# Performance work log

Measured on AMD Instinct MI355X. Metric: run time of the kernel, lower is better.

## Reference

```python
import jax, jax.numpy as jnp
import numpy as np

N_NODES = 50000
N_EDGES = 800000
VOCAB = 4096          # node_emb_size
EMB_DIM = 128         # node_emb_dim
HIDDEN = 128          # hidden_dim -> layer1 out = 2*HIDDEN
N_POS = 1024


def gcn_conv(h, edge_index, W, b, n):
    """PyG GCNConv: lin -> add self loops -> sym-normalized scatter-add -> +bias."""
    h = h @ W                                   # [N, out]
    row, col = edge_index[0], edge_index[1]     # source, target
    loop = jnp.arange(n)
    row = jnp.concatenate([row, loop])
    col = jnp.concatenate([col, loop])
    deg = jax.ops.segment_sum(jnp.ones(row.shape[0], dtype=h.dtype), col, num_segments=n)
    dinv = jnp.where(deg > 0, jax.lax.rsqrt(deg), 0.0)
    norm = dinv[row] * dinv[col]                # [E+N]
    msg = h[row] * norm[:, None]                # gather + scale
    return jax.ops.segment_sum(msg, col, num_segments=n) + b


def setup_inputs() -> dict:
    key = jax.random.key(0)
    ks = jax.random.split(key, 10)
    x = jax.random.randint(ks[0], (N_NODES, 1), 0, VOCAB)
    edge_index = jax.random.randint(ks[1], (2, N_EDGES), 0, N_NODES)
    x_position = jax.random.randint(ks[2], (N_POS,), 0, N_NODES)
    # Embedding init: normal(0, emb_dim^-0.5) per initialize_parameters
    emb = jax.random.normal(ks[3], (VOCAB, EMB_DIM), jnp.float32) * EMB_DIM ** -0.5
    # GCN / linear weights (glorot-ish)
    W1 = jax.random.normal(ks[4], (EMB_DIM, 2 * HIDDEN), jnp.float32) * (EMB_DIM ** -0.5)
    b1 = jnp.zeros((2 * HIDDEN,), jnp.float32)
    W2 = jax.random.normal(ks[5], (2 * HIDDEN, HIDDEN), jnp.float32) * ((2 * HIDDEN) ** -0.5)
    b2 = jnp.zeros((HIDDEN,), jnp.float32)
    Wc = jax.random.normal(ks[6], (HIDDEN, VOCAB), jnp.float32) * (HIDDEN ** -0.5)
    bc = jnp.zeros((VOCAB,), jnp.float32)
    return {"x": x, "edge_index": edge_index, "x_position": x_position,
            "emb": emb, "W1": W1, "b1": b1, "W2": W2, "b2": b2, "Wc": Wc, "bc": bc}


def reference(x, edge_index, x_position, emb, W1, b1, W2, b2, Wc, bc):
    n = x.shape[0]
    h = emb[x[:, 0]]                                   # Embedding + squeeze(1)
    h = jax.nn.relu(gcn_conv(h, edge_index, W1, b1, n))
    z = gcn_conv(h, edge_index, W2, b2, n)             # [N, HIDDEN]
    logits = z @ Wc + bc                               # classifier over all nodes
    # embedding stage: mean of classified rows at x_position, keep dim 0
    return jnp.mean(logits[x_position], axis=0, keepdims=True)  # [1, VOCAB]
```

## Files before the change

kernel.cpp:

```cpp
#include <hip/hip_runtime.h>

constexpr int EMB  = 128;
constexpr int H1D  = 256;
constexpr int H2D  = 128;
constexpr int VOC  = 4096;
constexpr int NSL  = 32;
constexpr int RPB  = 4;

constexpr int NRANGE = 8;
constexpr int TEAMS  = 64;
constexpr int RCAPW  = 3200;
constexpr int HIST_B = NRANGE * TEAMS;
constexpr int GEMM_B = VOC / RPB;
constexpr int KB_GRID = HIST_B + GEMM_B;

__global__ void kA_init(int* count, unsigned int* flagbits, unsigned int* needw,
                        float* wagg, float* wsum, int* nflag, int* total,
                        const int* __restrict__ xpos,
                        int n, int nwords, int np) {
    int t = threadIdx.x;
    if (blockIdx.x == 0) {
        for (int i = t; i < nwords; i += 256) flagbits[i] = 0u;
        for (int i = t; i < n; i += 256) count[i] = 0;
        __syncthreads();
        for (int i = t; i < np; i += 256) {
            int v = xpos[i];
            atomicAdd(&count[v], 1);
            atomicOr(&flagbits[v >> 5], 1u << (v & 31));
        }
        if (t == 0) { *nflag = 0; *total = 0; }
    } else {
        const int stride = (gridDim.x - 1) * 256;
        const int i0 = (blockIdx.x - 1) * 256 + t;
        for (int i = i0; i < n; i += stride) wagg[i] = 0.0f;
        for (int i = i0; i < nwords; i += stride) needw[i] = 0u;
        for (int i = i0; i < NSL * H1D; i += stride) wsum[i] = 0.0f;
    }
}

__global__ __launch_bounds__(256) void kB_embW1_hist(
        const float* __restrict__ emb, const float* __restrict__ W1,
        float* __restrict__ embW1,
        const int* __restrict__ row, const int* __restrict__ col,
        const unsigned int* __restrict__ flagbits,
        unsigned short* __restrict__ cntp16, unsigned int* markw,
        int ne, int R, int sTeam) {
    __shared__ unsigned int sbuf[RCAPW];
    int t = threadIdx.x;
    if (blockIdx.x < HIST_B) {
        int h     = blockIdx.x;
        int team  = h >> 3;
        int range = h & (NRANGE - 1);
        int base  = range * R;
        int RW    = R >> 1;
        for (int i = t; i < RW; i += 256) sbuf[i] = 0u;
        __syncthreads();
        int q  = (((ne + TEAMS - 1) / TEAMS) + 255) & ~255;
        int e0 = team * q;
        int e1 = min(ne, e0 + q);
        for (int e = e0 + t; e < e1; e += 256) {
            int c = col[e];
            unsigned int d = (unsigned int)(c - base);
            if (d < (unsigned int)R) {
                atomicAdd(&sbuf[d >> 1], 1u << ((d & 1) << 4));
                if ((flagbits[c >> 5] >> (c & 31)) & 1u) {
                    int r = row[e];
                    atomicOr(&markw[r >> 5], 1u << (r & 31));
                }
            }
        }
        __syncthreads();
        unsigned int* outp32 =
            (unsigned int*)(cntp16 + (size_t)team * sTeam + base);
        for (int i = t; i < RW; i += 256) outp32[i] = sbuf[i];
    } else {
        float (*er)[EMB] = (float (*)[EMB])sbuf;
        int r0 = (blockIdx.x - HIST_B) * RPB;
        for (int i = t; i < RPB * EMB; i += 256)
            er[i / EMB][i % EMB] = emb[(size_t)r0 * EMB + i];
        __syncthreads();
        float acc[RPB];
#pragma unroll
        for (int rr = 0; rr < RPB; rr++) acc[rr] = 0.0f;
        for (int k = 0; k < EMB; k++) {
            float w = W1[k * H1D + t];
#pragma unroll
            for (int rr = 0; rr < RPB; rr++) acc[rr] += er[rr][k] * w;
        }
#pragma unroll
        for (int rr = 0; rr < RPB; rr++)
            embW1[(size_t)(r0 + rr) * H1D + t] = acc[rr];
    }
}

__global__ void k_alloc(unsigned int* needw,
                        const unsigned int* __restrict__ flagbits,
                        const unsigned short* __restrict__ cntp16,
                        const int* __restrict__ count,
                        const int* __restrict__ x,
                        float* wagg, int* needlist, int* nflag, int* total,
                        int* offs, int* cursor, unsigned int* pkc, int* cnt,
                        int n, int sTeam) {
    int v = blockIdx.x * blockDim.x + threadIdx.x;
    int lane = threadIdx.x & 63;
    int cv = 0;
    bool need = false;
    if (v < n) {
        const unsigned short* cp = cntp16 + v;
#pragma unroll 8
        for (int tt = 0; tt < TEAMS; tt++) cv += cp[(size_t)tt * sTeam];
        cnt[v] = cv;
        pkc[v] = ((unsigned int)cv << 16) | (unsigned int)(x[v] & 0xFFFF);
        bool mark = (needw[v >> 5] >> (v & 31)) & 1u;
        bool flag = (flagbits[v >> 5] >> (v & 31)) & 1u;
        need = mark || flag;
        if (flag) wagg[v] = (float)count[v] / ((float)cv + 1.0f);
    }
    unsigned long long nm = __ballot(need);
    int wbase = (v & ~63) >> 5;
    if (lane == 0)  needw[wbase]     = (unsigned int)(nm & 0xffffffffu);
    if (lane == 32) needw[wbase + 1] = (unsigned int)(nm >> 32);
    int seg = need ? cv : 0;
    int incl = seg;
#pragma unroll
    for (int d = 1; d < 64; d <<= 1) {
        int t2 = __shfl_up(incl, d);
        if (lane >= d) incl += t2;
    }
    int excl = incl - seg;
    int wave_total = __shfl(incl, 63);
    int rank = __popcll(nm & ((1ull << lane) - 1));
    int wcnt = __popcll(nm);
    int base_id = 0, base_off = 0;
    if (lane == 0) {
        if (wcnt > 0)       base_id  = atomicAdd(nflag, wcnt);
        if (wave_total > 0) base_off = atomicAdd(total, wave_total);
    }
    base_id  = __shfl(base_id, 0);
    base_off = __shfl(base_off, 0);
    if (need) {
        needlist[base_id + rank] = v;
        int o = base_off + excl;
        offs[v] = o;
        cursor[v] = o;
    }
}

__global__ void k_scatter(const int* __restrict__ row, const int* __restrict__ col,
                          const unsigned int* __restrict__ needw,
                          const unsigned int* __restrict__ flagbits,
                          const int* __restrict__ count,
                          const unsigned int* __restrict__ pkc,
                          int* cursor, unsigned int* srow4, float* wagg, int ne) {
    int e = blockIdx.x * blockDim.x + threadIdx.x;
    if (e < ne) {
        int c = col[e];
        if ((needw[c >> 5] >> (c & 31)) & 1u) {
            int r = row[e];
            int pos = atomicAdd(&cursor[c], 1);
            unsigned int pr = pkc[r];
            srow4[pos] = pr;
            if ((flagbits[c >> 5] >> (c & 31)) & 1u) {
                float dr = rsqrtf((float)(pr >> 16) + 1.0f);
                float dc = rsqrtf((float)(pkc[c] >> 16) + 1.0f);
                atomicAdd(&wagg[r], (float)count[c] * dc * dr);
            }
        }
    }
}

__global__ void k_fconv(const int* __restrict__ needlist, const int* __restrict__ nneed_p,
                        const float* __restrict__ wagg, const int* __restrict__ x,
                        const unsigned int* __restrict__ srow4,
                        const int* __restrict__ offs, const int* __restrict__ cnt,
                        const float* __restrict__ embW1, const float* __restrict__ b1,
                        float* __restrict__ wsum) {
    int lane = threadIdx.x & 63;
    int wib  = threadIdx.x >> 6;
    int wid  = blockIdx.x * (blockDim.x >> 6) + wib;
    int nw   = gridDim.x * (blockDim.x >> 6);
    int nn   = *nneed_p;
    const float4* __restrict__ ew = (const float4*)embW1;
    float4 bfrag = ((const float4*)b1)[lane];
    float4 acc2 = {0.0f, 0.0f, 0.0f, 0.0f};

    for (int i = wid; i < nn; i += nw) {
        int v = needlist[i];
        int cv = cnt[v];
        float dv = rsqrtf((float)cv + 1.0f);
        float wa = wagg[v];
        float4 s = ew[(size_t)x[v] * 64 + lane];
        float w0 = dv * dv;
        float4 acc;
        acc.x = bfrag.x + w0 * s.x;
        acc.y = bfrag.y + w0 * s.y;
        acc.z = bfrag.z + w0 * s.z;
        acc.w = bfrag.w + w0 * s.w;
        int start = offs[v], m = cv;
        for (int base = 0; base < m; base += 64) {
            int mm = min(64, m - base);
            int xr = 0; float wr = 0.0f;
            if (lane < mm) {
                unsigned int pk2 = srow4[start + base + lane];
                xr = (int)(pk2 & 0xFFFFu);
                wr = rsqrtf((float)(pk2 >> 16) + 1.0f) * dv;
            }
            int e = 0;
            for (; e + 4 <= mm; e += 4) {
                int i0 = __shfl(xr, e),     i1 = __shfl(xr, e + 1);
                int i2 = __shfl(xr, e + 2), i3 = __shfl(xr, e + 3);
                float q0 = __shfl(wr, e),     q1 = __shfl(wr, e + 1);
                float q2 = __shfl(wr, e + 2), q3 = __shfl(wr, e + 3);
                float4 t0 = ew[(size_t)i0 * 64 + lane];
                float4 t1 = ew[(size_t)i1 * 64 + lane];
                float4 t2 = ew[(size_t)i2 * 64 + lane];
                float4 t3 = ew[(size_t)i3 * 64 + lane];
                acc.x += q0 * t0.x + q1 * t1.x + q2 * t2.x + q3 * t3.x;
                acc.y += q0 * t0.y + q1 * t1.y + q2 * t2.y + q3 * t3.y;
                acc.z += q0 * t0.z + q1 * t1.z + q2 * t2.z + q3 * t3.z;
                acc.w += q0 * t0.w + q1 * t1.w + q2 * t2.w + q3 * t3.w;
            }
            for (; e < mm; e++) {
                int i0 = __shfl(xr, e);
                float q0 = __shfl(wr, e);
                float4 t0 = ew[(size_t)i0 * 64 + lane];
                acc.x += q0 * t0.x;
                acc.y += q0 * t0.y;
                acc.z += q0 * t0.z;
                acc.w += q0 * t0.w;
            }
        }
        acc2.x += wa * fmaxf(acc.x, 0.0f);
        acc2.y += wa * fmaxf(acc.y, 0.0f);
        acc2.z += wa * fmaxf(acc.z, 0.0f);
        acc2.w += wa * fmaxf(acc.w, 0.0f);
    }

    __shared__ float red[4][H1D];
    red[wib][4 * lane + 0] = acc2.x;
    red[wib][4 * lane + 1] = acc2.y;
    red[wib][4 * lane + 2] = acc2.z;
    red[wib][4 * lane + 3] = acc2.w;
    __syncthreads();
    int t = threadIdx.x;
    float ssum = red[0][t] + red[1][t] + red[2][t] + red[3][t];
    atomicAdd(&wsum[(blockIdx.x & (NSL - 1)) * H1D + t], ssum);
}

__global__ void k_zout(const float* __restrict__ wsum, const float* __restrict__ W2,
                       const float* __restrict__ b2, const float* __restrict__ Wc,
                       const float* __restrict__ bc, float* __restrict__ out,
                       float inv_np) {
    __shared__ float ws[H1D];
    __shared__ float z[H2D];
    __shared__ float red[256];
    int t = threadIdx.x;
    float s = 0.0f;
#pragma unroll
    for (int c2 = 0; c2 < NSL; c2++) s += wsum[c2 * H1D + t];
    ws[t] = s;
    __syncthreads();
    if (t < H2D) {
        float acc = 0.0f;
#pragma unroll 8
        for (int k = 0; k < H1D; k++) acc += ws[k] * W2[k * H2D + t];
        z[t] = b2[t] + acc * inv_np;
    }
    __syncthreads();
    int c  = blockIdx.x * 16 + (t & 15);
    int js = t >> 4;
    float acc = 0.0f;
#pragma unroll
    for (int j = js * 8; j < js * 8 + 8; j++) acc += z[j] * Wc[(size_t)j * VOC + c];
    red[t] = acc;
    __syncthreads();
    if (t < 16) {
        int cc = blockIdx.x * 16 + t;
        float o = bc[cc];
#pragma unroll
        for (int ss = 0; ss < 16; ss++) o += red[ss * 16 + t];
        out[cc] = o;
    }
}

extern "C" void kernel_launch(void* const* d_in, const int* in_sizes, int n_in,
                              void* d_out, int out_size, void* d_ws, size_t ws_size,
                              hipStream_t stream) {
    const int n  = in_sizes[0];
    const int ne = in_sizes[1] / 2;
    const int np = in_sizes[2];

    const int*   x    = (const int*)d_in[0];
    const int*   ei   = (const int*)d_in[1];
    const int*   xpos = (const int*)d_in[2];
    const float* emb  = (const float*)d_in[3];
    const float* W1   = (const float*)d_in[4];
    const float* b1   = (const float*)d_in[5];
    const float* W2   = (const float*)d_in[6];
    const float* b2   = (const float*)d_in[7];
    const float* Wc   = (const float*)d_in[8];
    const float* bc   = (const float*)d_in[9];
    float*       out  = (float*)d_out;

    const int* row = ei;
    const int* col = ei + ne;

    char* p = (char*)d_ws;
    auto alloc = [&](size_t bytes) {
        char* r = p;
        p += (bytes + 255) & ~(size_t)255;
        return r;
    };
    const int nb     = (n + 255) / 256;
    const int neb    = (ne + 255) / 256;
    const int nwords = nb * 8;
    const int R      = (((n + NRANGE - 1) / NRANGE) + 1) & ~1;
    const int sTeam  = NRANGE * R;

    int*            cnt      = (int*)alloc((size_t)n * 4);
    int*            offs     = (int*)alloc((size_t)n * 4);
    int*            cursor   = (int*)alloc((size_t)n * 4);
    int*            count    = (int*)alloc((size_t)n * 4);
    int*            needlist = (int*)alloc((size_t)n * 4);
    unsigned int*   needw    = (unsigned int*)alloc((size_t)nwords * 4);
    unsigned int*   flagbits = (unsigned int*)alloc((size_t)nwords * 4);
    unsigned int*   srow4    = (unsigned int*)alloc((size_t)ne * 4);
    unsigned int*   pkc      = (unsigned int*)alloc((size_t)n * 4);
    unsigned short* cntp16   = (unsigned short*)alloc((size_t)TEAMS * sTeam * 2);
    int*            nflag    = (int*)alloc(256 * 4);
    int*            total    = (int*)alloc(256 * 4);
    float*          wagg     = (float*)alloc((size_t)n * 4);
    float*          embW1    = (float*)alloc((size_t)VOC * H1D * 4);
    float*          wsum     = (float*)alloc((size_t)NSL * H1D * 4);

    kA_init<<<nb, 256, 0, stream>>>(count, flagbits, needw, wagg, wsum,
                                    nflag, total, xpos, n, nwords, np);
    kB_embW1_hist<<<KB_GRID, 256, 0, stream>>>(emb, W1, embW1, row, col, flagbits,
                                               cntp16, needw, ne, R, sTeam);
    k_alloc<<<nb, 256, 0, stream>>>(needw, flagbits, cntp16, count, x, wagg,
                                    needlist, nflag, total, offs, cursor, pkc, cnt,
                                    n, sTeam);
    k_scatter<<<neb, 256, 0, stream>>>(row, col, needw, flagbits, count, pkc,
                                       cursor, srow4, wagg, ne);
    k_fconv<<<2048, 256, 0, stream>>>(needlist, nflag, wagg, x, srow4, offs, cnt,
                                      embW1, b1, wsum);
    k_zout<<<VOC / 16, 256, 0, stream>>>(wsum, W2, b2, Wc, bc, out, 1.0f / (float)np);
}
```

Measured before the change: 179.2 us.

## Widen histogram teams, use 32-bit LDS counters, tile W1 through shared memory

After: 172.0 us (median of 2 runs). -4.0%, faster.

```diff
diff --git a/kernel.cpp b/kernel.cpp
--- a/kernel.cpp
+++ b/kernel.cpp
@@ -6,10 +6,11 @@
 constexpr int VOC  = 4096;
 constexpr int NSL  = 32;
 constexpr int RPB  = 4;
+constexpr int KT   = 16;
 
 constexpr int NRANGE = 8;
-constexpr int TEAMS  = 64;
-constexpr int RCAPW  = 3200;
+constexpr int TEAMS  = 128;
+constexpr int RCAP   = 6400;
 constexpr int HIST_B = NRANGE * TEAMS;
 constexpr int GEMM_B = VOC / RPB;
 constexpr int KB_GRID = HIST_B + GEMM_B;
@@ -45,15 +46,14 @@
         const unsigned int* __restrict__ flagbits,
         unsigned short* __restrict__ cntp16, unsigned int* markw,
         int ne, int R, int sTeam) {
-    __shared__ unsigned int sbuf[RCAPW];
+    __shared__ unsigned int sbuf[RCAP];
     int t = threadIdx.x;
     if (blockIdx.x < HIST_B) {
         int h     = blockIdx.x;
         int team  = h >> 3;
         int range = h & (NRANGE - 1);
         int base  = range * R;
-        int RW    = R >> 1;
-        for (int i = t; i < RW; i += 256) sbuf[i] = 0u;
+        for (int i = t; i < R; i += 256) sbuf[i] = 0u;
         __syncthreads();
         int q  = (((ne + TEAMS - 1) / TEAMS) + 255) & ~255;
         int e0 = team * q;
@@ -62,7 +62,7 @@
             int c = col[e];
             unsigned int d = (unsigned int)(c - base);
             if (d < (unsigned int)R) {
-                atomicAdd(&sbuf[d >> 1], 1u << ((d & 1) << 4));
+                atomicAdd(&sbuf[d], 1u);
                 if ((flagbits[c >> 5] >> (c & 31)) & 1u) {
                     int r = row[e];
                     atomicOr(&markw[r >> 5], 1u << (r & 31));
@@ -70,22 +70,33 @@
             }
         }
         __syncthreads();
-        unsigned int* outp32 =
-            (unsigned int*)(cntp16 + (size_t)team * sTeam + base);
-        for (int i = t; i < RW; i += 256) outp32[i] = sbuf[i];
+        unsigned short* outp = cntp16 + (size_t)team * sTeam + base;
+        for (int i = t; i < R; i += 256) outp[i] = (unsigned short)sbuf[i];
     } else {
-        float (*er)[EMB] = (float (*)[EMB])sbuf;
+        float* sf = (float*)sbuf;
+        float (*er)[EMB]  = (float (*)[EMB])sf;
+        float (*w1t)[H1D] = (float (*)[H1D])(sf + RPB * EMB);
         int r0 = (blockIdx.x - HIST_B) * RPB;
-        for (int i = t; i < RPB * EMB; i += 256)
-            er[i / EMB][i % EMB] = emb[(size_t)r0 * EMB + i];
-        __syncthreads();
+        if (t < RPB * EMB / 4)
+            ((float4*)er)[t] = ((const float4*)(emb + (size_t)r0 * EMB))[t];
         float acc[RPB];
 #pragma unroll
         for (int rr = 0; rr < RPB; rr++) acc[rr] = 0.0f;
-        for (int k = 0; k < EMB; k++) {
-            float w = W1[k * H1D + t];
-#pragma unroll
-            for (int rr = 0; rr < RPB; rr++) acc[rr] += er[rr][k] * w;
+#pragma unroll
+        for (int kt = 0; kt < EMB / KT; kt++) {
+            __syncthreads();
+            const float4* w4 = (const float4*)(W1 + (size_t)kt * KT * H1D);
+#pragma unroll
+            for (int i = 0; i < KT * H1D / 4 / 256; i++)
+                ((float4*)w1t)[t + i * 256] = w4[t + i * 256];
+            __syncthreads();
+#pragma unroll
+            for (int k2 = 0; k2 < KT; k2++) {
+                float w = w1t[k2][t];
+                int k = kt * KT + k2;
+#pragma unroll
+                for (int rr = 0; rr < RPB; rr++) acc[rr] += er[rr][k] * w;
+            }
         }
 #pragma unroll
         for (int rr = 0; rr < RPB; rr++)
@@ -314,7 +325,7 @@
     const int nb     = (n + 255) / 256;
     const int neb    = (ne + 255) / 256;
     const int nwords = nb * 8;
-    const int R      = (((n + NRANGE - 1) / NRANGE) + 1) & ~1;
+    const int R      = (n + NRANGE - 1) / NRANGE;
     const int sTeam  = NRANGE * R;
 
     int*            cnt      = (int*)alloc((size_t)n * 4);
```
